# Performance work log

Hardware: AMD Instinct MI355X
Metric: run time of the kernel (lower is better)

The kernel has to match this reference:

```python
import jax, jax.numpy as jnp
import numpy as np
import math

# ---- static configuration (matches init_kwargs) ----
METADATA = [64, 48, 32]   # channels per l = 0,1,2
MAX_L = 3                 # order_out
N_BATCH = 32768
fact = math.factorial

def _cg_complex(l1, m1, l2, m2, l3, m3):
    # Clebsch-Gordan coefficient <l1 m1 l2 m2 | l3 m3> via Racah formula
    if m1 + m2 != m3 or l3 < abs(l1 - l2) or l3 > l1 + l2:
        return 0.0
    pre = math.sqrt((2*l3+1) * fact(l1+l2-l3) * fact(l1-l2+l3) * fact(-l1+l2+l3) / fact(l1+l2+l3+1))
    pre *= math.sqrt(fact(l1+m1)*fact(l1-m1)*fact(l2+m2)*fact(l2-m2)*fact(l3+m3)*fact(l3-m3))
    kmin = max(0, l2-l3-m1, l1-l3+m2)
    kmax = min(l1+l2-l3, l1-m1, l2+m2)
    s = 0.0
    for k in range(kmin, kmax+1):
        s += (-1)**k / (fact(k)*fact(l1+l2-l3-k)*fact(l1-m1-k)*fact(l2+m2-k)*fact(l3-l2+m1+k)*fact(l3-l1-m2+k))
    return pre * s

def _U(l):
    # complex->real spherical harmonic change of basis, rows = real m', cols = complex m
    U = np.zeros((2*l+1, 2*l+1), dtype=np.complex128)
    for m in range(-l, l+1):
        r = m + l
        if m > 0:
            U[r, m+l] = (-1)**m / math.sqrt(2.0); U[r, -m+l] = 1.0/math.sqrt(2.0)
        elif m == 0:
            U[r, l] = 1.0
        else:
            U[r, m+l] = 1j/math.sqrt(2.0); U[r, -m+l] = -1j*(-1)**m/math.sqrt(2.0)
    return U

def _real_cg(l1, l2, l3):
    Cc = np.zeros((2*l1+1, 2*l2+1, 2*l3+1))
    for m1 in range(-l1, l1+1):
        for m2 in range(-l2, l2+1):
            for m3 in range(-l3, l3+1):
                Cc[m1+l1, m2+l2, m3+l3] = _cg_complex(l1, m1, l2, m2, l3, m3)
    T = np.einsum('am,bn,co,mno->abc', _U(l1), _U(l2), _U(l3).conj(), Cc.astype(np.complex128))
    T = T.imag if np.abs(T.imag).max() > np.abs(T.real).max() else T.real
    return np.ascontiguousarray(T).astype(np.float32)

# ---- static index structures ----
L_IN = len(METADATA)
OFF_IN = np.concatenate([[0], np.cumsum([METADATA[l]*(2*l+1) for l in range(L_IN)])]).astype(np.int64)
DIM_IN = int(OFF_IN[-1])  # 368
PATHS = []
for l1 in range(L_IN):
    for l2 in range(L_IN):
        for l3 in range(abs(l1-l2), min(l1+l2, MAX_L)+1):
            PATHS.append((l1, l2, l3, min(METADATA[l1], METADATA[l2])))
MD_OV = [0]*(MAX_L+1)
for (_, _, l3, ch) in PATHS:
    MD_OV[l3] = max(MD_OV[l3], ch)
OFF_OUT = np.concatenate([[0], np.cumsum([MD_OV[l]*(2*l+1) for l in range(MAX_L+1)])]).astype(np.int64)
DIM_OUT = int(OFF_OUT[-1])  # 672
CG = {(l1, l2, l3): jnp.asarray(_real_cg(l1, l2, l3)) for (l1, l2, l3, _) in PATHS}

_mix_id, _scat = [], []
_base = 0
for (l1, l2, l3, ch) in PATHS:
    for i in range(ch):
        for m in range(2*l3+1):
            _mix_id.append(_base + i)
            _scat.append(int(OFF_OUT[l3]) + i*(2*l3+1) + m)
    _base += ch
MIX_ID = jnp.asarray(np.array(_mix_id, dtype=np.int64))
SCATTER = jnp.asarray(np.array(_scat, dtype=np.int64))
N_MIX = _base  # 688

_chan_in = []
_cb = 0
for l in range(L_IN):
    for i in range(METADATA[l]):
        _chan_in += [_cb + i]*(2*l+1)
    _cb += METADATA[l]
CHAN_IN = jnp.asarray(np.array(_chan_in, dtype=np.int64))
N_KEEP = _cb  # 144
_kin, _kout = [], []
for l in range(L_IN):
    cp = min(METADATA[l], MD_OV[l])
    for i in range(cp):
        for m in range(2*l+1):
            _kin.append(int(OFF_IN[l]) + i*(2*l+1) + m)
            _kout.append(int(OFF_OUT[l]) + i*(2*l+1) + m)
KEEP_IN = jnp.asarray(np.array(_kin, dtype=np.int64))
KEEP_OUT = jnp.asarray(np.array(_kout, dtype=np.int64))

SQ3 = math.sqrt(3.0)

def setup_inputs() -> dict:
    key = jax.random.key(0)
    k1, k2, k3 = jax.random.split(key, 3)
    x = jax.random.normal(k1, (N_BATCH, DIM_IN), dtype=jnp.float32)
    keep_coeff = jax.random.uniform(k2, (N_KEEP,), minval=-SQ3, maxval=SQ3, dtype=jnp.float32)
    mix_coeff = jax.random.uniform(k3, (N_MIX,), minval=-SQ3, maxval=SQ3, dtype=jnp.float32)
    return {"x": x, "keep_coeff": keep_coeff, "mix_coeff": mix_coeff}

def reference(x, keep_coeff, mix_coeff):
    n = x.shape[0]
    # keep path: per-channel coeff broadcast over m components
    x_keep = x * keep_coeff[CHAN_IN]  # [N, 368]
    # CG tensor-product self-coupling (diagonal channel pairing per path)
    tps = []
    for (l1, l2, l3, ch) in PATHS:
        x1 = x[:, OFF_IN[l1]:OFF_IN[l1]+ch*(2*l1+1)].reshape(n, ch, 2*l1+1)
        x2 = x[:, OFF_IN[l2]:OFF_IN[l2]+ch*(2*l2+1)].reshape(n, ch, 2*l2+1)
        tps.append(jnp.einsum('nia,nib,abm->nim', x1, x2, CG[(l1, l2, l3)]).reshape(n, -1))
    cat = jnp.concatenate(tps, axis=1)  # [N, 2576] non-overlapped TP output
    cat = cat * 0.5 * mix_coeff[MIX_ID]
    # scatter (index_add) into overlapped output layout
    out = jnp.zeros((n, DIM_OUT), dtype=x.dtype).at[:, SCATTER].add(cat)
    # gather + add of keep path (index_select + add_)
    out = out.at[:, KEEP_OUT].add(x_keep[:, KEEP_IN])
    return out
```

## Files before the change

### kernel.cpp

```cpp
#include <hip/hip_runtime.h>


namespace cgc {

struct cplx { double re, im; };
constexpr cplx cmul(cplx a, cplx b){ return {a.re*b.re - a.im*b.im, a.re*b.im + a.im*b.re}; }

constexpr double cfact(int n){ double r = 1.0; for (int i = 2; i <= n; ++i) r *= i; return r; }
constexpr double cabsd(double x){ return x < 0 ? -x : x; }

constexpr double csqrtd(double x){
  if (x <= 0.0) return 0.0;
  double g = x > 1.0 ? x : 1.0;
  for (int i = 0; i < 48; ++i) g = 0.5*(g + x/g);
  return g;
}

constexpr double SQRT2 = csqrtd(2.0);

constexpr double cg_complex(int l1,int m1,int l2,int m2,int l3,int m3){
  if (m1 + m2 != m3) return 0.0;
  int lo = l1 > l2 ? l1 - l2 : l2 - l1;
  if (l3 < lo || l3 > l1 + l2) return 0.0;
  double pre = csqrtd((2*l3+1) * cfact(l1+l2-l3)*cfact(l1-l2+l3)*cfact(-l1+l2+l3)/cfact(l1+l2+l3+1));
  pre *= csqrtd(cfact(l1+m1)*cfact(l1-m1)*cfact(l2+m2)*cfact(l2-m2)*cfact(l3+m3)*cfact(l3-m3));
  int kmin = 0;
  if (l2-l3-m1 > kmin) kmin = l2-l3-m1;
  if (l1-l3+m2 > kmin) kmin = l1-l3+m2;
  int kmax = l1+l2-l3;
  if (l1-m1 < kmax) kmax = l1-m1;
  if (l2+m2 < kmax) kmax = l2+m2;
  double s = 0.0;
  for (int k = kmin; k <= kmax; ++k){
    double d = cfact(k)*cfact(l1+l2-l3-k)*cfact(l1-m1-k)*cfact(l2+m2-k)
             * cfact(l3-l2+m1+k)*cfact(l3-l1-m2+k);
    s += ((k & 1) ? -1.0 : 1.0) / d;
  }
  return pre * s;
}

constexpr cplx Uent(int l, int r, int c){
  int m = r - l;
  if (m > 0){
    if (c ==  m + l) return { ((m & 1) ? -1.0 : 1.0)/SQRT2, 0.0 };
    if (c == -m + l) return { 1.0/SQRT2, 0.0 };
    return {0.0, 0.0};
  } else if (m == 0){
    if (c == l) return {1.0, 0.0};
    return {0.0, 0.0};
  } else {
    int ma = -m;
    if (c ==  m + l) return { 0.0, 1.0/SQRT2 };
    if (c == -m + l) return { 0.0, -(((ma & 1) ? -1.0 : 1.0))/SQRT2 };
    return {0.0, 0.0};
  }
}

template<int L1,int L2,int L3>
struct CGData { float w[(2*L1+1)*(2*L2+1)*(2*L3+1)]; };

template<int L1,int L2,int L3>
constexpr CGData<L1,L2,L3> make_cg(){
  constexpr int D1 = 2*L1+1, D2 = 2*L2+1, D3 = 2*L3+1;
  cplx U1[D1*D1] = {}; cplx U2[D2*D2] = {}; cplx U3c[D3*D3] = {};
  for (int r = 0; r < D1; ++r) for (int c = 0; c < D1; ++c) U1[r*D1+c] = Uent(L1, r, c);
  for (int r = 0; r < D2; ++r) for (int c = 0; c < D2; ++c) U2[r*D2+c] = Uent(L2, r, c);
  for (int r = 0; r < D3; ++r) for (int c = 0; c < D3; ++c){
    cplx u = Uent(L3, r, c); u.im = -u.im; U3c[r*D3+c] = u;
  }
  double Cc[D1*D2*D3] = {};
  for (int m1 = -L1; m1 <= L1; ++m1)
    for (int m2 = -L2; m2 <= L2; ++m2){
      int m3 = m1 + m2;
      if (m3 < -L3 || m3 > L3) continue;
      Cc[((m1+L1)*D2 + (m2+L2))*D3 + (m3+L3)] = cg_complex(L1,m1,L2,m2,L3,m3);
    }
  double re[D1*D2*D3] = {}; double im[D1*D2*D3] = {};
  for (int a = 0; a < D1; ++a)
    for (int b = 0; b < D2; ++b)
      for (int c = 0; c < D3; ++c){
        double sre = 0.0, sim = 0.0;
        for (int m = 0; m < D1; ++m)
          for (int n = 0; n < D2; ++n){
            int o = m + n - L1 - L2 + L3;
            if (o < 0 || o >= D3) continue;
            double cc = Cc[(m*D2+n)*D3 + o];
            if (cc == 0.0) continue;
            cplx p = cmul(cmul(U1[a*D1+m], U2[b*D2+n]), U3c[c*D3+o]);
            sre += p.re * cc; sim += p.im * cc;
          }
        re[(a*D2+b)*D3+c] = sre; im[(a*D2+b)*D3+c] = sim;
      }
  double mre = 0.0, mim = 0.0;
  for (int k = 0; k < D1*D2*D3; ++k){
    if (cabsd(re[k]) > mre) mre = cabsd(re[k]);
    if (cabsd(im[k]) > mim) mim = cabsd(im[k]);
  }
  CGData<L1,L2,L3> outv{};
  for (int k = 0; k < D1*D2*D3; ++k){
    double v = (mim > mre) ? im[k] : re[k];
    outv.w[k] = (cabsd(v) < 1e-10) ? 0.0f : (float)v;
  }
  return outv;
}

}

template<int L1,int L2,int L3>
__device__ __forceinline__ void tp_path(const float* xa, const float* xb, float cmix, float* acc){
  constexpr cgc::CGData<L1,L2,L3> cg = cgc::make_cg<L1,L2,L3>();
  constexpr int D1 = 2*L1+1, D2 = 2*L2+1, D3 = 2*L3+1;
  float tmp[D3];
  #pragma unroll
  for (int m = 0; m < D3; ++m) tmp[m] = 0.0f;
  #pragma unroll
  for (int a = 0; a < D1; ++a){
    #pragma unroll
    for (int b = 0; b < D2; ++b){
      const float pr = xa[a] * xb[b];
      #pragma unroll
      for (int m = 0; m < D3; ++m){
        const float W = cg.w[(a*D2+b)*D3 + m];
        if (W != 0.0f) tmp[m] += W * pr;
      }
    }
  }
  #pragma unroll
  for (int m = 0; m < D3; ++m) acc[m] += cmix * tmp[m];
}


__global__ __launch_bounds__(256) void selfmix_kernel(
    const float* __restrict__ x, const float* __restrict__ keep,
    const float* __restrict__ mix, float* __restrict__ out, int n)
{
  const long long gid = (long long)blockIdx.x * 256 + threadIdx.x;
  const long long nA = (long long)n * 32;
  const long long nB = (long long)n * 16;

  if (gid < nA){
    const int i   = (int)(gid & 31);
    const int row = (int)(gid >> 5);
    const float* xr = x + (long long)row * 368;
    float*     orow = out + (long long)row * 672;
    float s = xr[i];
    float p[3], d[5];
    #pragma unroll
    for (int k = 0; k < 3; ++k) p[k] = xr[64 + i*3 + k];
    #pragma unroll
    for (int k = 0; k < 5; ++k) d[k] = xr[208 + i*5 + k];

    float o0 = 0.f;
    float o1[3] = {0.f,0.f,0.f};
    float o2[5] = {0.f,0.f,0.f,0.f,0.f};
    float o3[7] = {0.f,0.f,0.f,0.f,0.f,0.f,0.f};

    tp_path<0,0,0>(&s,&s, 0.5f*mix[  0+i], &o0);
    tp_path<0,1,1>(&s, p, 0.5f*mix[ 64+i],  o1);
    tp_path<0,2,2>(&s, d, 0.5f*mix[112+i],  o2);
    tp_path<1,0,1>( p,&s, 0.5f*mix[144+i],  o1);
    tp_path<1,1,0>( p, p, 0.5f*mix[192+i], &o0);
    tp_path<1,1,1>( p, p, 0.5f*mix[240+i],  o1);
    tp_path<1,1,2>( p, p, 0.5f*mix[288+i],  o2);
    tp_path<1,2,1>( p, d, 0.5f*mix[336+i],  o1);
    tp_path<1,2,2>( p, d, 0.5f*mix[368+i],  o2);
    tp_path<1,2,3>( p, d, 0.5f*mix[400+i],  o3);
    tp_path<2,0,2>( d,&s, 0.5f*mix[432+i],  o2);
    tp_path<2,1,1>( d, p, 0.5f*mix[464+i],  o1);
    tp_path<2,1,2>( d, p, 0.5f*mix[496+i],  o2);
    tp_path<2,1,3>( d, p, 0.5f*mix[528+i],  o3);
    tp_path<2,2,0>( d, d, 0.5f*mix[560+i], &o0);
    tp_path<2,2,1>( d, d, 0.5f*mix[592+i],  o1);
    tp_path<2,2,2>( d, d, 0.5f*mix[624+i],  o2);
    tp_path<2,2,3>( d, d, 0.5f*mix[656+i],  o3);

    o0 += keep[i] * s;
    const float k1 = keep[64+i], k2 = keep[112+i];
    #pragma unroll
    for (int k = 0; k < 3; ++k) o1[k] += k1 * p[k];
    #pragma unroll
    for (int k = 0; k < 5; ++k) o2[k] += k2 * d[k];

    orow[i] = o0;
    #pragma unroll
    for (int k = 0; k < 3; ++k) orow[ 64 + i*3 + k] = o1[k];
    #pragma unroll
    for (int k = 0; k < 5; ++k) orow[208 + i*5 + k] = o2[k];
    #pragma unroll
    for (int k = 0; k < 7; ++k) orow[448 + i*7 + k] = o3[k];

  } else if (gid < nA + nB){
    const long long t = gid - nA;
    const int i   = 32 + (int)(t & 15);
    const int row = (int)(t >> 4);
    const float* xr = x + (long long)row * 368;
    float*     orow = out + (long long)row * 672;
    float s = xr[i];
    float p[3];
    #pragma unroll
    for (int k = 0; k < 3; ++k) p[k] = xr[64 + i*3 + k];

    float o0 = 0.f;
    float o1[3] = {0.f,0.f,0.f};
    float o2[5] = {0.f,0.f,0.f,0.f,0.f};

    tp_path<0,0,0>(&s,&s, 0.5f*mix[  0+i], &o0);
    tp_path<0,1,1>(&s, p, 0.5f*mix[ 64+i],  o1);
    tp_path<1,0,1>( p,&s, 0.5f*mix[144+i],  o1);
    tp_path<1,1,0>( p, p, 0.5f*mix[192+i], &o0);
    tp_path<1,1,1>( p, p, 0.5f*mix[240+i],  o1);
    tp_path<1,1,2>( p, p, 0.5f*mix[288+i],  o2);

    o0 += keep[i] * s;
    const float k1 = keep[64+i];
    #pragma unroll
    for (int k = 0; k < 3; ++k) o1[k] += k1 * p[k];

    orow[i] = o0;
    #pragma unroll
    for (int k = 0; k < 3; ++k) orow[ 64 + i*3 + k] = o1[k];
    #pragma unroll
    for (int k = 0; k < 5; ++k) orow[208 + i*5 + k] = o2[k];

  } else if (gid < nA + 2*nB){
    const long long t = gid - nA - nB;
    const int i   = 48 + (int)(t & 15);
    const int row = (int)(t >> 4);
    const float* xr = x + (long long)row * 368;
    float s = xr[i];
    float o0 = 0.f;
    tp_path<0,0,0>(&s,&s, 0.5f*mix[0+i], &o0);
    o0 += keep[i] * s;
    out[(long long)row * 672 + i] = o0;
  }
}

extern "C" void kernel_launch(void* const* d_in, const int* in_sizes, int n_in,
                              void* d_out, int out_size, void* d_ws, size_t ws_size,
                              hipStream_t stream)
{
  const float* x    = (const float*)d_in[0];
  const float* keep = (const float*)d_in[1];
  const float* mix  = (const float*)d_in[2];
  float* out = (float*)d_out;
  const int n = in_sizes[0] / 368;
  const long long total = (long long)n * 64;
  const int blocks = (int)((total + 255) / 256);
  selfmix_kernel<<<blocks, 256, 0, stream>>>(x, keep, mix, out, n);
}
```

Measured before the change: 137.2 us.

## Stage input rows and output segments through shared memory with float4 coalescing

Channels 0-31 are now handled by blocks of eight rows each. A block loads all eight input rows into LDS with coalesced float4 reads, computes from LDS, then writes its output segments back to LDS and stores them to global memory as float4 at remapped offsets. This replaces the strided per-thread loads and stores of l=1, l=2 and l=3 components, which were poorly coalesced. It adds two extra barriers and 16KB of LDS per block, which may reduce occupancy. The channel 32-63 branches keep direct global access.

```diff
diff --git a/kernel.cpp b/kernel.cpp
--- a/kernel.cpp
+++ b/kernel.cpp
@@ -134,21 +134,40 @@
     const float* __restrict__ x, const float* __restrict__ keep,
     const float* __restrict__ mix, float* __restrict__ out, int n)
 {
-  const long long gid = (long long)blockIdx.x * 256 + threadIdx.x;
-  const long long nA = (long long)n * 32;
-  const long long nB = (long long)n * 16;
-
-  if (gid < nA){
-    const int i   = (int)(gid & 31);
-    const int row = (int)(gid >> 5);
-    const float* xr = x + (long long)row * 368;
-    float*     orow = out + (long long)row * 672;
-    float s = xr[i];
-    float p[3], d[5];
-    #pragma unroll
-    for (int k = 0; k < 3; ++k) p[k] = xr[64 + i*3 + k];
-    #pragma unroll
-    for (int k = 0; k < 5; ++k) d[k] = xr[208 + i*5 + k];
+  __shared__ __align__(16) float buf[8 * 512];
+
+  const int t   = threadIdx.x;
+  const int blk = blockIdx.x;
+  const int bA  = (n + 7)  >> 3;
+  const int bB  = (n + 15) >> 4;
+
+  if (blk < bA){
+    const long long row0 = (long long)blk * 8;
+    float4* buf4 = (float4*)buf;
+
+    {
+      const long long nf4 = (long long)n * 92;
+      const long long base = row0 * 92;
+      const float4* __restrict__ x4 = (const float4*)x;
+      if (base + t < nf4)              buf4[t]       = x4[base + t];
+      if (base + 256 + t < nf4)        buf4[256 + t] = x4[base + 256 + t];
+      if (t < 224 && base + 512 + t < nf4) buf4[512 + t] = x4[base + 512 + t];
+    }
+    __syncthreads();
+
+    const int rowL = t >> 5;
+    const int i    = t & 31;
+    const bool live = (row0 + rowL) < n;
+
+    float s = 0.f, p[3] = {0.f,0.f,0.f}, d[5] = {0.f,0.f,0.f,0.f,0.f};
+    if (live){
+      const float* xr = buf + rowL * 368;
+      s = xr[i];
+      #pragma unroll
+      for (int k = 0; k < 3; ++k) p[k] = xr[64 + i*3 + k];
+      #pragma unroll
+      for (int k = 0; k < 5; ++k) d[k] = xr[208 + i*5 + k];
+    }
 
     float o0 = 0.f;
     float o1[3] = {0.f,0.f,0.f};
@@ -181,57 +200,82 @@
     #pragma unroll
     for (int k = 0; k < 5; ++k) o2[k] += k2 * d[k];
 
-    orow[i] = o0;
-    #pragma unroll
-    for (int k = 0; k < 3; ++k) orow[ 64 + i*3 + k] = o1[k];
-    #pragma unroll
-    for (int k = 0; k < 5; ++k) orow[208 + i*5 + k] = o2[k];
-    #pragma unroll
-    for (int k = 0; k < 7; ++k) orow[448 + i*7 + k] = o3[k];
-
-  } else if (gid < nA + nB){
-    const long long t = gid - nA;
-    const int i   = 32 + (int)(t & 15);
-    const int row = (int)(t >> 4);
-    const float* xr = x + (long long)row * 368;
-    float*     orow = out + (long long)row * 672;
-    float s = xr[i];
-    float p[3];
-    #pragma unroll
-    for (int k = 0; k < 3; ++k) p[k] = xr[64 + i*3 + k];
-
-    float o0 = 0.f;
-    float o1[3] = {0.f,0.f,0.f};
-    float o2[5] = {0.f,0.f,0.f,0.f,0.f};
-
-    tp_path<0,0,0>(&s,&s, 0.5f*mix[  0+i], &o0);
-    tp_path<0,1,1>(&s, p, 0.5f*mix[ 64+i],  o1);
-    tp_path<1,0,1>( p,&s, 0.5f*mix[144+i],  o1);
-    tp_path<1,1,0>( p, p, 0.5f*mix[192+i], &o0);
-    tp_path<1,1,1>( p, p, 0.5f*mix[240+i],  o1);
-    tp_path<1,1,2>( p, p, 0.5f*mix[288+i],  o2);
-
-    o0 += keep[i] * s;
-    const float k1 = keep[64+i];
-    #pragma unroll
-    for (int k = 0; k < 3; ++k) o1[k] += k1 * p[k];
-
-    orow[i] = o0;
-    #pragma unroll
-    for (int k = 0; k < 3; ++k) orow[ 64 + i*3 + k] = o1[k];
-    #pragma unroll
-    for (int k = 0; k < 5; ++k) orow[208 + i*5 + k] = o2[k];
-
-  } else if (gid < nA + 2*nB){
-    const long long t = gid - nA - nB;
-    const int i   = 48 + (int)(t & 15);
-    const int row = (int)(t >> 4);
-    const float* xr = x + (long long)row * 368;
-    float s = xr[i];
-    float o0 = 0.f;
-    tp_path<0,0,0>(&s,&s, 0.5f*mix[0+i], &o0);
-    o0 += keep[i] * s;
-    out[(long long)row * 672 + i] = o0;
+    __syncthreads();
+
+    if (live){
+      float* orw = buf + rowL * 512;
+      orw[i] = o0;
+      #pragma unroll
+      for (int k = 0; k < 3; ++k) orw[ 32 + i*3 + k] = o1[k];
+      #pragma unroll
+      for (int k = 0; k < 5; ++k) orw[128 + i*5 + k] = o2[k];
+      #pragma unroll
+      for (int k = 0; k < 7; ++k) orw[288 + i*7 + k] = o3[k];
+    }
+    __syncthreads();
+
+    {
+      const float4* bo4 = (const float4*)buf;
+      float4* __restrict__ o4 = (float4*)out;
+      #pragma unroll
+      for (int rnd = 0; rnd < 4; ++rnd){
+        const int sidx = rnd*256 + t;
+        const int r = sidx >> 7;
+        const int k = sidx & 127;
+        const long long row = row0 + r;
+        if (row < n){
+          const int g = k + (k < 8 ? 0 : (k < 32 ? 8 : (k < 72 ? 20 : 40)));
+          o4[row*168 + g] = bo4[sidx];
+        }
+      }
+    }
+
+  } else if (blk < bA + bB){
+    const long long t2 = (long long)(blk - bA) * 256 + t;
+    const int i        = 32 + (int)(t2 & 15);
+    const long long row = t2 >> 4;
+    if (row < n){
+      const float* xr = x + row * 368;
+      float*     orow = out + row * 672;
+      float s = xr[i];
+      float p[3];
+      #pragma unroll
+      for (int k = 0; k < 3; ++k) p[k] = xr[64 + i*3 + k];
+
+      float o0 = 0.f;
+      float o1[3] = {0.f,0.f,0.f};
+      float o2[5] = {0.f,0.f,0.f,0.f,0.f};
+
+      tp_path<0,0,0>(&s,&s, 0.5f*mix[  0+i], &o0);
+      tp_path<0,1,1>(&s, p, 0.5f*mix[ 64+i],  o1);
+      tp_path<1,0,1>( p,&s, 0.5f*mix[144+i],  o1);
+      tp_path<1,1,0>( p, p, 0.5f*mix[192+i], &o0);
+      tp_path<1,1,1>( p, p, 0.5f*mix[240+i],  o1);
+      tp_path<1,1,2>( p, p, 0.5f*mix[288+i],  o2);
+
+      o0 += keep[i] * s;
+      const float k1 = keep[64+i];
+      #pragma unroll
+      for (int k = 0; k < 3; ++k) o1[k] += k1 * p[k];
+
+      orow[i] = o0;
+      #pragma unroll
+      for (int k = 0; k < 3; ++k) orow[ 64 + i*3 + k] = o1[k];
+      #pragma unroll
+      for (int k = 0; k < 5; ++k) orow[208 + i*5 + k] = o2[k];
+    }
+
+  } else {
+    const long long t2 = (long long)(blk - bA - bB) * 256 + t;
+    const int i        = 48 + (int)(t2 & 15);
+    const long long row = t2 >> 4;
+    if (row < n){
+      float s = x[row * 368 + i];
+      float o0 = 0.f;
+      tp_path<0,0,0>(&s,&s, 0.5f*mix[0+i], &o0);
+      o0 += keep[i] * s;
+      out[row * 672 + i] = o0;
+    }
   }
 }
 
@@ -243,8 +287,9 @@
   const float* keep = (const float*)d_in[1];
   const float* mix  = (const float*)d_in[2];
   float* out = (float*)d_out;
-  const int n = in_sizes[0] / 368;
-  const long long total = (long long)n * 64;
-  const int blocks = (int)((total + 255) / 256);
+  const int n  = in_sizes[0] / 368;
+  const int bA = (n + 7)  >> 3;
+  const int bB = (n + 15) >> 4;
+  const int blocks = bA + 2 * bB;
   selfmix_kernel<<<blocks, 256, 0, stream>>>(x, keep, mix, out, n);
 }
```

New measurement: 135.1 us. No clear change (-1.6%).

## Stage input rows in LDS via float4 loads and give each block eight rows

Applied to the files above, without the earlier changes.

Each 256-thread block now handles 8 rows. Each wave copies its own two input rows into shared memory with coalesced float4 loads, then computes from shared memory. This replaces the strided per-thread scalar global reads of the l=1 and l=2 components. Each lane now does one heavy l≤2 channel and one lighter channel for the remaining 32 channels, so the grid is smaller and per-thread work is more even. There is no barrier between the shared-memory write and read, which relies on each wave reading only the rows it loaded itself. Output stores stay strided.

```diff
diff --git a/kernel.cpp b/kernel.cpp
--- a/kernel.cpp
+++ b/kernel.cpp
@@ -134,104 +134,122 @@
     const float* __restrict__ x, const float* __restrict__ keep,
     const float* __restrict__ mix, float* __restrict__ out, int n)
 {
-  const long long gid = (long long)blockIdx.x * 256 + threadIdx.x;
-  const long long nA = (long long)n * 32;
-  const long long nB = (long long)n * 16;
-
-  if (gid < nA){
-    const int i   = (int)(gid & 31);
-    const int row = (int)(gid >> 5);
-    const float* xr = x + (long long)row * 368;
-    float*     orow = out + (long long)row * 672;
-    float s = xr[i];
-    float p[3], d[5];
-    #pragma unroll
-    for (int k = 0; k < 3; ++k) p[k] = xr[64 + i*3 + k];
-    #pragma unroll
-    for (int k = 0; k < 5; ++k) d[k] = xr[208 + i*5 + k];
-
-    float o0 = 0.f;
-    float o1[3] = {0.f,0.f,0.f};
-    float o2[5] = {0.f,0.f,0.f,0.f,0.f};
-    float o3[7] = {0.f,0.f,0.f,0.f,0.f,0.f,0.f};
-
-    tp_path<0,0,0>(&s,&s, 0.5f*mix[  0+i], &o0);
-    tp_path<0,1,1>(&s, p, 0.5f*mix[ 64+i],  o1);
-    tp_path<0,2,2>(&s, d, 0.5f*mix[112+i],  o2);
-    tp_path<1,0,1>( p,&s, 0.5f*mix[144+i],  o1);
-    tp_path<1,1,0>( p, p, 0.5f*mix[192+i], &o0);
-    tp_path<1,1,1>( p, p, 0.5f*mix[240+i],  o1);
-    tp_path<1,1,2>( p, p, 0.5f*mix[288+i],  o2);
-    tp_path<1,2,1>( p, d, 0.5f*mix[336+i],  o1);
-    tp_path<1,2,2>( p, d, 0.5f*mix[368+i],  o2);
-    tp_path<1,2,3>( p, d, 0.5f*mix[400+i],  o3);
-    tp_path<2,0,2>( d,&s, 0.5f*mix[432+i],  o2);
-    tp_path<2,1,1>( d, p, 0.5f*mix[464+i],  o1);
-    tp_path<2,1,2>( d, p, 0.5f*mix[496+i],  o2);
-    tp_path<2,1,3>( d, p, 0.5f*mix[528+i],  o3);
-    tp_path<2,2,0>( d, d, 0.5f*mix[560+i], &o0);
-    tp_path<2,2,1>( d, d, 0.5f*mix[592+i],  o1);
-    tp_path<2,2,2>( d, d, 0.5f*mix[624+i],  o2);
-    tp_path<2,2,3>( d, d, 0.5f*mix[656+i],  o3);
-
-    o0 += keep[i] * s;
-    const float k1 = keep[64+i], k2 = keep[112+i];
-    #pragma unroll
-    for (int k = 0; k < 3; ++k) o1[k] += k1 * p[k];
-    #pragma unroll
-    for (int k = 0; k < 5; ++k) o2[k] += k2 * d[k];
-
-    orow[i] = o0;
-    #pragma unroll
-    for (int k = 0; k < 3; ++k) orow[ 64 + i*3 + k] = o1[k];
-    #pragma unroll
-    for (int k = 0; k < 5; ++k) orow[208 + i*5 + k] = o2[k];
-    #pragma unroll
-    for (int k = 0; k < 7; ++k) orow[448 + i*7 + k] = o3[k];
-
-  } else if (gid < nA + nB){
-    const long long t = gid - nA;
-    const int i   = 32 + (int)(t & 15);
-    const int row = (int)(t >> 4);
-    const float* xr = x + (long long)row * 368;
-    float*     orow = out + (long long)row * 672;
-    float s = xr[i];
-    float p[3];
-    #pragma unroll
-    for (int k = 0; k < 3; ++k) p[k] = xr[64 + i*3 + k];
-
-    float o0 = 0.f;
-    float o1[3] = {0.f,0.f,0.f};
-    float o2[5] = {0.f,0.f,0.f,0.f,0.f};
-
-    tp_path<0,0,0>(&s,&s, 0.5f*mix[  0+i], &o0);
-    tp_path<0,1,1>(&s, p, 0.5f*mix[ 64+i],  o1);
-    tp_path<1,0,1>( p,&s, 0.5f*mix[144+i],  o1);
-    tp_path<1,1,0>( p, p, 0.5f*mix[192+i], &o0);
-    tp_path<1,1,1>( p, p, 0.5f*mix[240+i],  o1);
-    tp_path<1,1,2>( p, p, 0.5f*mix[288+i],  o2);
-
-    o0 += keep[i] * s;
-    const float k1 = keep[64+i];
-    #pragma unroll
-    for (int k = 0; k < 3; ++k) o1[k] += k1 * p[k];
-
-    orow[i] = o0;
-    #pragma unroll
-    for (int k = 0; k < 3; ++k) orow[ 64 + i*3 + k] = o1[k];
-    #pragma unroll
-    for (int k = 0; k < 5; ++k) orow[208 + i*5 + k] = o2[k];
-
-  } else if (gid < nA + 2*nB){
-    const long long t = gid - nA - nB;
-    const int i   = 48 + (int)(t & 15);
-    const int row = (int)(t >> 4);
-    const float* xr = x + (long long)row * 368;
-    float s = xr[i];
-    float o0 = 0.f;
-    tp_path<0,0,0>(&s,&s, 0.5f*mix[0+i], &o0);
-    o0 += keep[i] * s;
-    out[(long long)row * 672 + i] = o0;
+  __shared__ __align__(16) float xs[8 * 368];
+
+  const int t = threadIdx.x;
+  const int w = t >> 6;
+  const int l = t & 63;
+  const long long g    = blockIdx.x;
+  const long long row0 = g * 8;
+
+  const float4* __restrict__ x4 = (const float4*)x;
+  float4* xs4 = (float4*)xs;
+  const long long nf4i = (long long)n * 92;
+
+  {
+    const long long b  = g * 736 + (long long)w * 184;
+    const int       sb = w * 184;
+    if (b + l       < nf4i) xs4[sb + l]       = x4[b + l];
+    if (b + 64 + l  < nf4i) xs4[sb + 64 + l]  = x4[b + 64 + l];
+    if (l < 56 && b + 128 + l < nf4i) xs4[sb + 128 + l] = x4[b + 128 + l];
+  }
+
+  {
+    const int rowL = w*2 + (l >> 5);
+    const int i    = l & 31;
+    if (row0 + rowL < n){
+      const float* xr   = xs + rowL * 368;
+      float*       orow = out + (row0 + rowL) * 672;
+      float s = xr[i];
+      float p[3], d[5];
+      #pragma unroll
+      for (int k = 0; k < 3; ++k) p[k] = xr[64 + i*3 + k];
+      #pragma unroll
+      for (int k = 0; k < 5; ++k) d[k] = xr[208 + i*5 + k];
+
+      float o0 = 0.f;
+      float o1[3] = {0.f,0.f,0.f};
+      float o2[5] = {0.f,0.f,0.f,0.f,0.f};
+      float o3[7] = {0.f,0.f,0.f,0.f,0.f,0.f,0.f};
+
+      tp_path<0,0,0>(&s,&s, 0.5f*mix[  0+i], &o0);
+      tp_path<0,1,1>(&s, p, 0.5f*mix[ 64+i],  o1);
+      tp_path<0,2,2>(&s, d, 0.5f*mix[112+i],  o2);
+      tp_path<1,0,1>( p,&s, 0.5f*mix[144+i],  o1);
+      tp_path<1,1,0>( p, p, 0.5f*mix[192+i], &o0);
+      tp_path<1,1,1>( p, p, 0.5f*mix[240+i],  o1);
+      tp_path<1,1,2>( p, p, 0.5f*mix[288+i],  o2);
+      tp_path<1,2,1>( p, d, 0.5f*mix[336+i],  o1);
+      tp_path<1,2,2>( p, d, 0.5f*mix[368+i],  o2);
+      tp_path<1,2,3>( p, d, 0.5f*mix[400+i],  o3);
+      tp_path<2,0,2>( d,&s, 0.5f*mix[432+i],  o2);
+      tp_path<2,1,1>( d, p, 0.5f*mix[464+i],  o1);
+      tp_path<2,1,2>( d, p, 0.5f*mix[496+i],  o2);
+      tp_path<2,1,3>( d, p, 0.5f*mix[528+i],  o3);
+      tp_path<2,2,0>( d, d, 0.5f*mix[560+i], &o0);
+      tp_path<2,2,1>( d, d, 0.5f*mix[592+i],  o1);
+      tp_path<2,2,2>( d, d, 0.5f*mix[624+i],  o2);
+      tp_path<2,2,3>( d, d, 0.5f*mix[656+i],  o3);
+
+      o0 += keep[i] * s;
+      const float k1 = keep[64+i], k2 = keep[112+i];
+      #pragma unroll
+      for (int k = 0; k < 3; ++k) o1[k] += k1 * p[k];
+      #pragma unroll
+      for (int k = 0; k < 5; ++k) o2[k] += k2 * d[k];
+
+      orow[i] = o0;
+      #pragma unroll
+      for (int k = 0; k < 3; ++k) orow[ 64 + i*3 + k] = o1[k];
+      #pragma unroll
+      for (int k = 0; k < 5; ++k) orow[208 + i*5 + k] = o2[k];
+      #pragma unroll
+      for (int k = 0; k < 7; ++k) orow[448 + i*7 + k] = o3[k];
+    }
+  }
+
+  {
+    const int rowL = w*2 + ((l >> 4) & 1);
+    if (row0 + rowL < n){
+      if (l < 32){
+        const int i = 32 + (l & 15);
+        const float* xr   = xs + rowL * 368;
+        float*       orow = out + (row0 + rowL) * 672;
+        float s = xr[i];
+        float p[3];
+        #pragma unroll
+        for (int k = 0; k < 3; ++k) p[k] = xr[64 + i*3 + k];
+
+        float o0 = 0.f;
+        float o1[3] = {0.f,0.f,0.f};
+        float o2[5] = {0.f,0.f,0.f,0.f,0.f};
+
+        tp_path<0,0,0>(&s,&s, 0.5f*mix[  0+i], &o0);
+        tp_path<0,1,1>(&s, p, 0.5f*mix[ 64+i],  o1);
+        tp_path<1,0,1>( p,&s, 0.5f*mix[144+i],  o1);
+        tp_path<1,1,0>( p, p, 0.5f*mix[192+i], &o0);
+        tp_path<1,1,1>( p, p, 0.5f*mix[240+i],  o1);
+        tp_path<1,1,2>( p, p, 0.5f*mix[288+i],  o2);
+
+        o0 += keep[i] * s;
+        const float k1 = keep[64+i];
+        #pragma unroll
+        for (int k = 0; k < 3; ++k) o1[k] += k1 * p[k];
+
+        orow[i] = o0;
+        #pragma unroll
+        for (int k = 0; k < 3; ++k) orow[ 64 + i*3 + k] = o1[k];
+        #pragma unroll
+        for (int k = 0; k < 5; ++k) orow[208 + i*5 + k] = o2[k];
+      } else {
+        const int i = 48 + (l & 15);
+        const float s = xs[rowL*368 + i];
+        float o0 = 0.f;
+        tp_path<0,0,0>(&s,&s, 0.5f*mix[0+i], &o0);
+        o0 += keep[i] * s;
+        out[(row0 + rowL) * 672 + i] = o0;
+      }
+    }
   }
 }
 
@@ -244,7 +262,6 @@
   const float* mix  = (const float*)d_in[2];
   float* out = (float*)d_out;
   const int n = in_sizes[0] / 368;
-  const long long total = (long long)n * 64;
-  const int blocks = (int)((total + 255) / 256);
+  const int blocks = (n + 7) / 8;
   selfmix_kernel<<<blocks, 256, 0, stream>>>(x, keep, mix, out, n);
 }
```

Measured after the change: 136.8 us. Within noise of the previous version (-0.3%).
